# Optimization experiments

Measured on AMD Instinct MI355X. Metric: run time of the kernel, lower is better.

The kernel has to match this reference:

```python
import jax, jax.numpy as jnp
import numpy as np


def setup_inputs() -> dict:
    key = jax.random.key(0)
    ks = jax.random.split(key, 7)
    C, Cq = 128, 16  # channels, channels//8
    B, H, W = 8, 64, 64
    s = 0.05
    return {
        "x": jax.random.normal(ks[0], (B, C, H, W), jnp.float32),
        "wq": jax.random.normal(ks[1], (Cq, C), jnp.float32) * s,
        "bq": jnp.zeros((Cq,), jnp.float32),
        "wk": jax.random.normal(ks[2], (Cq, C), jnp.float32) * s,
        "bk": jnp.zeros((Cq,), jnp.float32),
        "wv": jax.random.normal(ks[3], (C, C), jnp.float32) * s,
        "bv": jnp.zeros((C,), jnp.float32),
    }


def reference(x, wq, bq, wk, bk, wv, bv):
    B, C, H, W = x.shape
    N = H * W
    dk = wq.shape[0]  # channels // 8
    xf = x.reshape(B, C, N)  # [B, C, N]
    # 1x1 convs == per-pixel linear maps over channels
    q = jnp.einsum('oc,bcn->bon', wq, xf) + bq[None, :, None]  # [B, dk, N]
    k = jnp.einsum('oc,bcn->bon', wk, xf) + bk[None, :, None]  # [B, dk, N]
    v = jnp.einsum('oc,bcn->bon', wv, xf) + bv[None, :, None]  # [B, C, N]
    # scores[b,i,j] = <q[:,i], k[:,j]> / sqrt(dk)
    scores = jnp.einsum('bdi,bdj->bij', q, k) / jnp.sqrt(jnp.asarray(dk, x.dtype))
    attn = jax.nn.softmax(scores, axis=-1)  # softmax over key dim j
    # out[b,c,i] = sum_j v[b,c,j] * attn[b,i,j]
    out = jnp.einsum('bcj,bij->bci', v, attn)
    return out.reshape(B, C, H, W) + x
```

## Files before the change

kernel.cpp:

```cpp
#include <hip/hip_runtime.h>
#include <hip/hip_bf16.h>

#define BATCH 8
#define CDIM  128
#define DK    16
#define NPIX  4096

typedef __attribute__((ext_vector_type(4)))  float    f32x4;
typedef __attribute__((ext_vector_type(16))) float    f32x16;
typedef __attribute__((ext_vector_type(8)))  short    s16x8;
typedef __attribute__((ext_vector_type(4)))  unsigned u32x4;

__device__ __forceinline__ short f2bf(float f) {
    union { float fv; unsigned u; } un; un.fv = f;
    unsigned r = un.u + 0x7FFFu + ((un.u >> 16) & 1u);
    return (short)(r >> 16);
}
__device__ __forceinline__ float bf2f(short s) {
    union { unsigned u; float f; } un; un.u = ((unsigned)(unsigned short)s) << 16;
    return un.f;
}
__device__ __forceinline__ float fexp2(float x) {
#if __has_builtin(__builtin_amdgcn_exp2f)
    return __builtin_amdgcn_exp2f(x);
#else
    return exp2f(x);
#endif
}
__device__ __forceinline__ unsigned pkbf(float lo, float hi) {
    __hip_bfloat162 h = __float22bfloat162_rn(make_float2(lo, hi));
    return *reinterpret_cast<unsigned*>(&h);
}
__device__ __forceinline__ f32x16 zero16() {
    f32x16 z;
    #pragma unroll
    for (int i = 0; i < 16; ++i) z[i] = 0.f;
    return z;
}

#define C2F 0.36067376022224085f
#define WPFRAGS (10 * 4 * 64)

__global__ __launch_bounds__(256) void wprep(
    const float* __restrict__ wq, const float* __restrict__ wk,
    const float* __restrict__ wv, short* __restrict__ Wp)
{
    const int mt   = blockIdx.x;
    const int t    = threadIdx.x;
    const int kt   = t >> 6;
    const int lane = t & 63;
    const int m    = mt * 16 + (lane & 15);
    const int c0   = kt * 32 + ((lane >> 4) << 3);

    const float* src; float scl = 1.f;
    if (m < 16)      { src = wq + m * CDIM; scl = C2F; }
    else if (m < 32) { src = wk + (m - 16) * CDIM; }
    else             { src = wv + (m - 32) * CDIM; }

    s16x8 frag;
    #pragma unroll
    for (int i = 0; i < 8; ++i) frag[i] = f2bf(src[c0 + i] * scl);
    *(s16x8*)(Wp + (((size_t)(mt * 4 + kt) * 64 + lane) << 3)) = frag;
}

__global__ __launch_bounds__(256) void qkv_proj(
    const float* __restrict__ x, const short* __restrict__ Wp,
    const float* __restrict__ bq, const float* __restrict__ bk,
    const float* __restrict__ bv,
    short* __restrict__ Qt, short* __restrict__ Kt, short* __restrict__ Vp)
{
    const int tid   = threadIdx.x;
    const int bid   = blockIdx.x;
    const int b     = bid >> 6;
    const int nbase = (bid & 63) << 6;

    const int lane = tid & 63;
    const int lo   = lane & 15;
    const int hi   = lane >> 4;
    const int n    = ((tid >> 6) << 4) + lo;
    const int ng   = nbase + n;

    const float* xb = x + (((size_t)(b * CDIM)) << 12) + ng;

    s16x8 bfr[4];
    #pragma unroll
    for (int kt = 0; kt < 4; ++kt) {
        const float* xp = xb + (((size_t)(kt * 32 + hi * 8)) << 12);
        float v0 = xp[0];
        float v1 = xp[(size_t)1 << 12];
        float v2 = xp[(size_t)2 << 12];
        float v3 = xp[(size_t)3 << 12];
        float v4 = xp[(size_t)4 << 12];
        float v5 = xp[(size_t)5 << 12];
        float v6 = xp[(size_t)6 << 12];
        float v7 = xp[(size_t)7 << 12];
        union { u32x4 u; s16x8 v; } pk;
        pk.u[0] = pkbf(v0, v1); pk.u[1] = pkbf(v2, v3);
        pk.u[2] = pkbf(v4, v5); pk.u[3] = pkbf(v6, v7);
        bfr[kt] = pk.v;
    }

    f32x4 acc[10];
    #pragma unroll
    for (int mt = 0; mt < 10; ++mt) { acc[mt][0]=0.f; acc[mt][1]=0.f; acc[mt][2]=0.f; acc[mt][3]=0.f; }

    #pragma unroll
    for (int kt = 0; kt < 4; ++kt) {
        #pragma unroll
        for (int mt = 0; mt < 10; ++mt) {
            const s16x8 af = *(const s16x8*)(Wp + (((size_t)(mt * 4 + kt) * 64 + lane) << 3));
            acc[mt] = __builtin_amdgcn_mfma_f32_16x16x32_bf16(af, bfr[kt], acc[mt], 0, 0, 0);
        }
    }

    const int m4 = hi << 2;
    {
        uint2 pk;
        pk.x = pkbf(acc[0][0] + bq[m4 + 0] * C2F, acc[0][1] + bq[m4 + 1] * C2F);
        pk.y = pkbf(acc[0][2] + bq[m4 + 2] * C2F, acc[0][3] + bq[m4 + 3] * C2F);
        *(uint2*)(Qt + ((((size_t)(b << 12)) + ng) << 4) + m4) = pk;
    }
    {
        uint2 pk;
        pk.x = pkbf(acc[1][0] + bk[m4 + 0], acc[1][1] + bk[m4 + 1]);
        pk.y = pkbf(acc[1][2] + bk[m4 + 2], acc[1][3] + bk[m4 + 3]);
        *(uint2*)(Kt + ((((size_t)(b << 12)) + ng) << 4) + m4) = pk;
    }
    {
        short* vpb = Vp + ((((size_t)(b * 64 + (ng >> 6)) * 8 + ((ng >> 3) & 7)) * 128) << 3)
                        + (ng & 7);
        #pragma unroll
        for (int mt = 2; mt < 10; ++mt) {
            #pragma unroll
            for (int r = 0; r < 4; ++r) {
                const int c = (mt - 2) * 16 + m4 + r;
                vpb[c << 3] = f2bf(acc[mt][r] + bv[c]);
            }
        }
    }
}

template<int KSPLIT, bool DIRECT>
__global__ __launch_bounds__(256, 4) void attn_part(
    const short* __restrict__ Qt, const short* __restrict__ Kt,
    const short* __restrict__ Vp, const float* __restrict__ x,
    float* __restrict__ out, short* __restrict__ Op, float* __restrict__ lsum)
{
    constexpr int NKEY = NPIX / KSPLIT;
    constexpr int NT   = NKEY / 64;

    const int tid = threadIdx.x;
    const int bid = blockIdx.x;
    const int b   = bid & 7;
    const int qb  = (bid >> 3) & 31;
    const int kc  = bid >> 8;
    const int q0  = qb * 128 + (tid >> 6) * 32;
    const int l31 = tid & 31;
    const int hi2 = (tid >> 5) & 1;
    const int kq  = hi2 << 3;
    const int pi  = (l31 & ~12) | ((l31 & 4) << 1) | ((l31 & 8) >> 1);

    const s16x8 qB = *(const s16x8*)(Qt + (((size_t)(b << 12) + q0 + l31) << 4) + kq);

    const int jbase0 = kc * NKEY;
    const short* ktb = Kt + ((size_t)(b << 12) << 4);
    const short* vX = Vp + (((size_t)(b * 64) * 8 * 128) << 3) + (l31 << 3);

    f32x16 O0 = zero16(), O1 = zero16(), O2 = zero16(), O3 = zero16();
    float l_acc = 0.f;

    #define KLOAD(jb) (*(const s16x8*)(ktb + (((size_t)((jb) + pi)) << 4) + kq))
    #define VFRAG(tg, ch, ct) (*(const s16x8*)(vX + ((size_t)(((tg) * 8 + (ch)) << 10) + ((ct) << 8))))
    #define LOADVF(dst, tg, h) do {                          \
        const int ch_ = ((h) << 1) | hi2;                    \
        dst[0] = VFRAG(tg, ch_, 0);                          \
        dst[1] = VFRAG(tg, ch_, 1);                          \
        dst[2] = VFRAG(tg, ch_, 2);                          \
        dst[3] = VFRAG(tg, ch_, 3);                          \
    } while (0)

    #define HALFP(sv, ktl, vf) do {                                             \
        float p0 = fexp2(sv[8*(ktl)+0]), p1 = fexp2(sv[8*(ktl)+1]);            \
        float p2 = fexp2(sv[8*(ktl)+2]), p3 = fexp2(sv[8*(ktl)+3]);            \
        float p4 = fexp2(sv[8*(ktl)+4]), p5 = fexp2(sv[8*(ktl)+5]);            \
        float p6 = fexp2(sv[8*(ktl)+6]), p7 = fexp2(sv[8*(ktl)+7]);            \
        l_acc += ((p0+p1)+(p2+p3)) + ((p4+p5)+(p6+p7));                        \
        union { u32x4 u; s16x8 v; } pc_;                                       \
        pc_.u[0] = pkbf(p0,p1); pc_.u[1] = pkbf(p2,p3);                        \
        pc_.u[2] = pkbf(p4,p5); pc_.u[3] = pkbf(p6,p7);                        \
        __builtin_amdgcn_s_setprio(1);                                          \
        O0 = __builtin_amdgcn_mfma_f32_32x32x16_bf16(vf[0], pc_.v, O0, 0,0,0); \
        O1 = __builtin_amdgcn_mfma_f32_32x32x16_bf16(vf[1], pc_.v, O1, 0,0,0); \
        O2 = __builtin_amdgcn_mfma_f32_32x32x16_bf16(vf[2], pc_.v, O2, 0,0,0); \
        O3 = __builtin_amdgcn_mfma_f32_32x32x16_bf16(vf[3], pc_.v, O3, 0,0,0); \
        __builtin_amdgcn_s_setprio(0);                                          \
    } while (0)

    for (int t = 0; t < NT; ++t) {
        const int jb = jbase0 + (t << 6);
        const int tg = jb >> 6;

        s16x8 vf[4];
        const s16x8 kA0 = KLOAD(jb);
        f32x16 s0 = __builtin_amdgcn_mfma_f32_32x32x16_bf16(kA0, qB, zero16(), 0, 0, 0);
        LOADVF(vf, tg, 0);
        HALFP(s0, 0, vf);
        LOADVF(vf, tg, 1);
        HALFP(s0, 1, vf);

        const s16x8 kA1 = KLOAD(jb + 32);
        f32x16 s1 = __builtin_amdgcn_mfma_f32_32x32x16_bf16(kA1, qB, zero16(), 0, 0, 0);
        LOADVF(vf, tg, 2);
        HALFP(s1, 0, vf);
        LOADVF(vf, tg, 3);
        HALFP(s1, 1, vf);
    }

    float l_tot = l_acc + __shfl_xor(l_acc, 32);
    const int ncol = q0 + l31;

    if constexpr (DIRECT) {
        const float inv = 1.f / l_tot;
        #define EPID(Ov, ct) do {                                              \
            _Pragma("unroll")                                                  \
            for (int r = 0; r < 16; ++r) {                                     \
                const int c = (ct)*32 + (r&3) + 8*(r>>2) + (hi2<<2);           \
                const size_t off = (((size_t)(b * CDIM + c)) << 12) + ncol;    \
                out[off] = Ov[r] * inv + x[off];                               \
            } } while (0)
        EPID(O0, 0); EPID(O1, 1); EPID(O2, 2); EPID(O3, 3);
    } else {
        const int prow = (kc * 8 + b) * CDIM;
        #define EPIP(Ov, ct) do {                                              \
            _Pragma("unroll")                                                  \
            for (int r = 0; r < 16; ++r) {                                     \
                const int c = (ct)*32 + (r&3) + 8*(r>>2) + (hi2<<2);           \
                Op[(((size_t)(prow + c)) << 12) + ncol] = f2bf(Ov[r]);         \
            } } while (0)
        EPIP(O0, 0); EPIP(O1, 1); EPIP(O2, 2); EPIP(O3, 3);
        if (!hi2) lsum[(((size_t)(kc * 8 + b)) << 12) + ncol] = l_tot;
    }
}

template<int KSPLIT>
__global__ __launch_bounds__(256) void attn_combine(
    const short* __restrict__ Op, const float* __restrict__ lsum,
    const float* __restrict__ x, float* __restrict__ out)
{
    __shared__ float linv[256];
    const int tid = threadIdx.x;
    const int bid = blockIdx.x;
    const int b   = bid >> 7;
    const int nb  = (bid >> 3) & 15;
    const int cb  = bid & 7;
    const int nbase = nb << 8;

    {
        float s = 0.f;
        #pragma unroll
        for (int k = 0; k < KSPLIT; ++k)
            s += lsum[(((size_t)(k * 8 + b)) << 12) + nbase + tid];
        linv[tid] = 1.f / s;
    }
    __syncthreads();

    const int n8 = (tid & 31) << 3;
    #pragma unroll
    for (int pass = 0; pass < 2; ++pass) {
        const int c = (cb << 4) + (pass << 3) + (tid >> 5);
        const size_t gbase = (((size_t)(b * CDIM + c)) << 12) + nbase + n8;
        float acc[8];
        #pragma unroll
        for (int j = 0; j < 8; ++j) acc[j] = 0.f;
        #pragma unroll
        for (int k = 0; k < KSPLIT; ++k) {
            s16x8 v = *(const s16x8*)(Op + (((size_t)((k * 8 + b) * CDIM + c)) << 12) + nbase + n8);
            #pragma unroll
            for (int j = 0; j < 8; ++j) acc[j] += bf2f(v[j]);
        }
        float4 li0 = *(const float4*)&linv[n8];
        float4 li1 = *(const float4*)&linv[n8 + 4];
        float4 x0  = *(const float4*)(x + gbase);
        float4 x1  = *(const float4*)(x + gbase + 4);
        float4 o0, o1;
        o0.x = acc[0] * li0.x + x0.x;  o0.y = acc[1] * li0.y + x0.y;
        o0.z = acc[2] * li0.z + x0.z;  o0.w = acc[3] * li0.w + x0.w;
        o1.x = acc[4] * li1.x + x1.x;  o1.y = acc[5] * li1.y + x1.y;
        o1.z = acc[6] * li1.z + x1.z;  o1.w = acc[7] * li1.w + x1.w;
        *(float4*)(out + gbase)     = o0;
        *(float4*)(out + gbase + 4) = o1;
    }
}

extern "C" void kernel_launch(void* const* d_in, const int* in_sizes, int n_in,
                              void* d_out, int out_size, void* d_ws, size_t ws_size,
                              hipStream_t stream) {
    const float* x  = (const float*)d_in[0];
    const float* wq = (const float*)d_in[1];
    const float* bq = (const float*)d_in[2];
    const float* wk = (const float*)d_in[3];
    const float* bk = (const float*)d_in[4];
    const float* wv = (const float*)d_in[5];
    const float* bv = (const float*)d_in[6];
    float* out = (float*)d_out;

    short* Qt = (short*)d_ws;
    short* Kt = Qt + (size_t)BATCH * NPIX * DK;
    short* Vp = Kt + (size_t)BATCH * NPIX * DK;
    short* Wpk = Vp + (size_t)BATCH * CDIM * NPIX;
    char*  extra = (char*)(Wpk + (size_t)WPFRAGS * 8);
    const size_t used    = (size_t)(extra - (char*)d_ws);
    const size_t opBytes = (size_t)BATCH * CDIM * NPIX * sizeof(short);
    const size_t lBytes  = (size_t)BATCH * NPIX * sizeof(float);

    wprep<<<dim3(10), dim3(256), 0, stream>>>(wq, wk, wv, Wpk);
    qkv_proj<<<dim3(512), dim3(256), 0, stream>>>(x, Wpk, bq, bk, bv, Qt, Kt, Vp);

    if (used + 4 * (opBytes + lBytes) <= ws_size) {
        short* Opw = (short*)extra;
        float* ls  = (float*)(extra + 4 * opBytes);
        attn_part<4, false><<<dim3(8 * 32 * 4), dim3(256), 0, stream>>>(Qt, Kt, Vp, x, out, Opw, ls);
        attn_combine<4><<<dim3(1024), dim3(256), 0, stream>>>(Opw, ls, x, out);
    } else if (used + 2 * (opBytes + lBytes) <= ws_size) {
        short* Opw = (short*)extra;
        float* ls  = (float*)(extra + 2 * opBytes);
        attn_part<2, false><<<dim3(8 * 32 * 2), dim3(256), 0, stream>>>(Qt, Kt, Vp, x, out, Opw, ls);
        attn_combine<2><<<dim3(1024), dim3(256), 0, stream>>>(Opw, ls, x, out);
    } else {
        attn_part<1, true><<<dim3(8 * 32), dim3(256), 0, stream>>>(Qt, Kt, Vp, x, out, nullptr, nullptr);
    }
}
```

Before: 84.41 us.

## Switch attention kernel from 32x32x16 to 16x16x32 MFMA with 16-query waves

Rewrites the attention partial kernel to use 16x16x32 bf16 MFMA instead of 32x32x16. Each wave now handles 16 queries instead of 32, so the grid doubles. QK^T zero-pads the upper K lanes because DK is only 16, which wastes half of each score MFMA. The exp/pack and PV loops are reorganized into 8 channel tiles of 4-wide accumulators, with incremental pointers for K and V. The aim is lower register pressure and better MFMA issue, at the cost of padded score compute and more V reloads per query.

```diff
diff --git a/kernel.cpp b/kernel.cpp
--- a/kernel.cpp
+++ b/kernel.cpp
@@ -7,7 +7,6 @@
 #define NPIX  4096
 
 typedef __attribute__((ext_vector_type(4)))  float    f32x4;
-typedef __attribute__((ext_vector_type(16))) float    f32x16;
 typedef __attribute__((ext_vector_type(8)))  short    s16x8;
 typedef __attribute__((ext_vector_type(4)))  unsigned u32x4;
 
@@ -30,12 +29,6 @@
 __device__ __forceinline__ unsigned pkbf(float lo, float hi) {
     __hip_bfloat162 h = __float22bfloat162_rn(make_float2(lo, hi));
     return *reinterpret_cast<unsigned*>(&h);
-}
-__device__ __forceinline__ f32x16 zero16() {
-    f32x16 z;
-    #pragma unroll
-    for (int i = 0; i < 16; ++i) z[i] = 0.f;
-    return z;
 }
 
 #define C2F 0.36067376022224085f
@@ -152,93 +145,99 @@
     const int tid = threadIdx.x;
     const int bid = blockIdx.x;
     const int b   = bid & 7;
-    const int qb  = (bid >> 3) & 31;
-    const int kc  = bid >> 8;
-    const int q0  = qb * 128 + (tid >> 6) * 32;
-    const int l31 = tid & 31;
-    const int hi2 = (tid >> 5) & 1;
-    const int kq  = hi2 << 3;
-    const int pi  = (l31 & ~12) | ((l31 & 4) << 1) | ((l31 & 8) >> 1);
-
-    const s16x8 qB = *(const s16x8*)(Qt + (((size_t)(b << 12) + q0 + l31) << 4) + kq);
-
+    const int qb  = (bid >> 3) & 63;
+    const int kc  = bid >> 9;
+    const int wv  = tid >> 6;
+    const int lane = tid & 63;
+    const int lo  = lane & 15;
+    const int hi  = lane >> 4;
+    const int q0  = qb * 64 + wv * 16;
+
+    s16x8 qB;
+    #pragma unroll
+    for (int i = 0; i < 8; ++i) qB[i] = 0;
+    if (hi < 2)
+        qB = *(const s16x8*)(Qt + (((size_t)(b << 12) + q0 + lo) << 4) + hi * 8);
+
+    const int pk0 = ((lo >> 2) << 3) + (lo & 3);
     const int jbase0 = kc * NKEY;
-    const short* ktb = Kt + ((size_t)(b << 12) << 4);
-    const short* vX = Vp + (((size_t)(b * 64) * 8 * 128) << 3) + (l31 << 3);
-
-    f32x16 O0 = zero16(), O1 = zero16(), O2 = zero16(), O3 = zero16();
+
+    const short* kb = Kt + (((size_t)(b << 12) + jbase0 + pk0) << 4) + hi * 8;
+    const short* vb = Vp + (size_t)b * 524288 + (size_t)(jbase0 >> 6) * 8192 + lo * 8;
+
+    f32x4 O[8];
+    #pragma unroll
+    for (int ct = 0; ct < 8; ++ct) { O[ct][0]=0.f; O[ct][1]=0.f; O[ct][2]=0.f; O[ct][3]=0.f; }
     float l_acc = 0.f;
-
-    #define KLOAD(jb) (*(const s16x8*)(ktb + (((size_t)((jb) + pi)) << 4) + kq))
-    #define VFRAG(tg, ch, ct) (*(const s16x8*)(vX + ((size_t)(((tg) * 8 + (ch)) << 10) + ((ct) << 8))))
-    #define LOADVF(dst, tg, h) do {                          \
-        const int ch_ = ((h) << 1) | hi2;                    \
-        dst[0] = VFRAG(tg, ch_, 0);                          \
-        dst[1] = VFRAG(tg, ch_, 1);                          \
-        dst[2] = VFRAG(tg, ch_, 2);                          \
-        dst[3] = VFRAG(tg, ch_, 3);                          \
-    } while (0)
-
-    #define HALFP(sv, ktl, vf) do {                                             \
-        float p0 = fexp2(sv[8*(ktl)+0]), p1 = fexp2(sv[8*(ktl)+1]);            \
-        float p2 = fexp2(sv[8*(ktl)+2]), p3 = fexp2(sv[8*(ktl)+3]);            \
-        float p4 = fexp2(sv[8*(ktl)+4]), p5 = fexp2(sv[8*(ktl)+5]);            \
-        float p6 = fexp2(sv[8*(ktl)+6]), p7 = fexp2(sv[8*(ktl)+7]);            \
-        l_acc += ((p0+p1)+(p2+p3)) + ((p4+p5)+(p6+p7));                        \
-        union { u32x4 u; s16x8 v; } pc_;                                       \
-        pc_.u[0] = pkbf(p0,p1); pc_.u[1] = pkbf(p2,p3);                        \
-        pc_.u[2] = pkbf(p4,p5); pc_.u[3] = pkbf(p6,p7);                        \
-        __builtin_amdgcn_s_setprio(1);                                          \
-        O0 = __builtin_amdgcn_mfma_f32_32x32x16_bf16(vf[0], pc_.v, O0, 0,0,0); \
-        O1 = __builtin_amdgcn_mfma_f32_32x32x16_bf16(vf[1], pc_.v, O1, 0,0,0); \
-        O2 = __builtin_amdgcn_mfma_f32_32x32x16_bf16(vf[2], pc_.v, O2, 0,0,0); \
-        O3 = __builtin_amdgcn_mfma_f32_32x32x16_bf16(vf[3], pc_.v, O3, 0,0,0); \
-        __builtin_amdgcn_s_setprio(0);                                          \
-    } while (0)
+    const f32x4 z4 = {0.f, 0.f, 0.f, 0.f};
 
     for (int t = 0; t < NT; ++t) {
-        const int jb = jbase0 + (t << 6);
-        const int tg = jb >> 6;
-
-        s16x8 vf[4];
-        const s16x8 kA0 = KLOAD(jb);
-        f32x16 s0 = __builtin_amdgcn_mfma_f32_32x32x16_bf16(kA0, qB, zero16(), 0, 0, 0);
-        LOADVF(vf, tg, 0);
-        HALFP(s0, 0, vf);
-        LOADVF(vf, tg, 1);
-        HALFP(s0, 1, vf);
-
-        const s16x8 kA1 = KLOAD(jb + 32);
-        f32x16 s1 = __builtin_amdgcn_mfma_f32_32x32x16_bf16(kA1, qB, zero16(), 0, 0, 0);
-        LOADVF(vf, tg, 2);
-        HALFP(s1, 0, vf);
-        LOADVF(vf, tg, 3);
-        HALFP(s1, 1, vf);
-    }
-
-    float l_tot = l_acc + __shfl_xor(l_acc, 32);
-    const int ncol = q0 + l31;
+        const s16x8 k0 = *(const s16x8*)(kb);
+        const s16x8 k1 = *(const s16x8*)(kb + (4  << 4));
+        const s16x8 k2 = *(const s16x8*)(kb + (32 << 4));
+        const s16x8 k3 = *(const s16x8*)(kb + (36 << 4));
+        f32x4 s0 = __builtin_amdgcn_mfma_f32_16x16x32_bf16(k0, qB, z4, 0, 0, 0);
+        f32x4 s1 = __builtin_amdgcn_mfma_f32_16x16x32_bf16(k1, qB, z4, 0, 0, 0);
+        f32x4 s2 = __builtin_amdgcn_mfma_f32_16x16x32_bf16(k2, qB, z4, 0, 0, 0);
+        f32x4 s3 = __builtin_amdgcn_mfma_f32_16x16x32_bf16(k3, qB, z4, 0, 0, 0);
+
+        union { u32x4 u; s16x8 v; } pc0, pc1;
+        {
+            float a0 = fexp2(s0[0]), a1 = fexp2(s0[1]), a2 = fexp2(s0[2]), a3 = fexp2(s0[3]);
+            float c0 = fexp2(s1[0]), c1 = fexp2(s1[1]), c2 = fexp2(s1[2]), c3 = fexp2(s1[3]);
+            l_acc += ((a0 + a1) + (a2 + a3)) + ((c0 + c1) + (c2 + c3));
+            pc0.u[0] = pkbf(a0, a1); pc0.u[1] = pkbf(a2, a3);
+            pc0.u[2] = pkbf(c0, c1); pc0.u[3] = pkbf(c2, c3);
+        }
+        {
+            float a0 = fexp2(s2[0]), a1 = fexp2(s2[1]), a2 = fexp2(s2[2]), a3 = fexp2(s2[3]);
+            float c0 = fexp2(s3[0]), c1 = fexp2(s3[1]), c2 = fexp2(s3[2]), c3 = fexp2(s3[3]);
+            l_acc += ((a0 + a1) + (a2 + a3)) + ((c0 + c1) + (c2 + c3));
+            pc1.u[0] = pkbf(a0, a1); pc1.u[1] = pkbf(a2, a3);
+            pc1.u[2] = pkbf(c0, c1); pc1.u[3] = pkbf(c2, c3);
+        }
+
+        __builtin_amdgcn_s_setprio(1);
+        #pragma unroll
+        for (int ct = 0; ct < 8; ++ct) {
+            const s16x8 v0 = *(const s16x8*)(vb + (size_t)(hi    ) * 1024 + ct * 128);
+            const s16x8 v1 = *(const s16x8*)(vb + (size_t)(hi + 4) * 1024 + ct * 128);
+            O[ct] = __builtin_amdgcn_mfma_f32_16x16x32_bf16(v0, pc0.v, O[ct], 0, 0, 0);
+            O[ct] = __builtin_amdgcn_mfma_f32_16x16x32_bf16(v1, pc1.v, O[ct], 0, 0, 0);
+        }
+        __builtin_amdgcn_s_setprio(0);
+
+        kb += 1024;
+        vb += 8192;
+    }
+
+    float l_tot = l_acc;
+    l_tot += __shfl_xor(l_tot, 16);
+    l_tot += __shfl_xor(l_tot, 32);
+    const int ncol = q0 + lo;
 
     if constexpr (DIRECT) {
         const float inv = 1.f / l_tot;
-        #define EPID(Ov, ct) do {                                              \
-            _Pragma("unroll")                                                  \
-            for (int r = 0; r < 16; ++r) {                                     \
-                const int c = (ct)*32 + (r&3) + 8*(r>>2) + (hi2<<2);           \
-                const size_t off = (((size_t)(b * CDIM + c)) << 12) + ncol;    \
-                out[off] = Ov[r] * inv + x[off];                               \
-            } } while (0)
-        EPID(O0, 0); EPID(O1, 1); EPID(O2, 2); EPID(O3, 3);
+        #pragma unroll
+        for (int ct = 0; ct < 8; ++ct) {
+            #pragma unroll
+            for (int r = 0; r < 4; ++r) {
+                const int c = ct * 16 + hi * 4 + r;
+                const size_t off = (((size_t)(b * CDIM + c)) << 12) + ncol;
+                out[off] = O[ct][r] * inv + x[off];
+            }
+        }
     } else {
         const int prow = (kc * 8 + b) * CDIM;
-        #define EPIP(Ov, ct) do {                                              \
-            _Pragma("unroll")                                                  \
-            for (int r = 0; r < 16; ++r) {                                     \
-                const int c = (ct)*32 + (r&3) + 8*(r>>2) + (hi2<<2);           \
-                Op[(((size_t)(prow + c)) << 12) + ncol] = f2bf(Ov[r]);         \
-            } } while (0)
-        EPIP(O0, 0); EPIP(O1, 1); EPIP(O2, 2); EPIP(O3, 3);
-        if (!hi2) lsum[(((size_t)(kc * 8 + b)) << 12) + ncol] = l_tot;
+        #pragma unroll
+        for (int ct = 0; ct < 8; ++ct) {
+            #pragma unroll
+            for (int r = 0; r < 4; ++r) {
+                const int c = ct * 16 + hi * 4 + r;
+                Op[(((size_t)(prow + c)) << 12) + ncol] = f2bf(O[ct][r]);
+            }
+        }
+        if (hi == 0) lsum[(((size_t)(kc * 8 + b)) << 12) + ncol] = l_tot;
     }
 }
 
@@ -319,14 +318,14 @@
     if (used + 4 * (opBytes + lBytes) <= ws_size) {
         short* Opw = (short*)extra;
         float* ls  = (float*)(extra + 4 * opBytes);
-        attn_part<4, false><<<dim3(8 * 32 * 4), dim3(256), 0, stream>>>(Qt, Kt, Vp, x, out, Opw, ls);
+        attn_part<4, false><<<dim3(8 * 64 * 4), dim3(256), 0, stream>>>(Qt, Kt, Vp, x, out, Opw, ls);
         attn_combine<4><<<dim3(1024), dim3(256), 0, stream>>>(Opw, ls, x, out);
     } else if (used + 2 * (opBytes + lBytes) <= ws_size) {
         short* Opw = (short*)extra;
         float* ls  = (float*)(extra + 2 * opBytes);
-        attn_part<2, false><<<dim3(8 * 32 * 2), dim3(256), 0, stream>>>(Qt, Kt, Vp, x, out, Opw, ls);
+        attn_part<2, false><<<dim3(8 * 64 * 2), dim3(256), 0, stream>>>(Qt, Kt, Vp, x, out, Opw, ls);
         attn_combine<2><<<dim3(1024), dim3(256), 0, stream>>>(Opw, ls, x, out);
     } else {
-        attn_part<1, true><<<dim3(8 * 32), dim3(256), 0, stream>>>(Qt, Kt, Vp, x, out, nullptr, nullptr);
-    }
-}
+        attn_part<1, true><<<dim3(8 * 64), dim3(256), 0, stream>>>(Qt, Kt, Vp, x, out, nullptr, nullptr);
+    }
+}
```

Result: slower. 120.1 us, median of 2 (+42.3%).
